# Performance work log

Measured on AMD Instinct MI355X. Metric: run time of the kernel, lower is better.

Reference implementation:

```python
import jax, jax.numpy as jnp
import numpy as np

EMB_DIM = 1024
NUM_HEADS = 16
HEAD_DIM = EMB_DIM // NUM_HEADS
B, S_Q, S_KV = 4, 2048, 2048


def setup_inputs() -> dict:
    key = jax.random.key(0)
    ks = jax.random.split(key, 12)
    s = EMB_DIM ** -0.5  # torch Linear default init scale (approx, uniform-like)
    inp = {
        "q": jax.random.normal(ks[0], (B, S_Q, EMB_DIM), jnp.float32),
        "k": jax.random.normal(ks[1], (B, S_KV, EMB_DIM), jnp.float32),
        "v": jax.random.normal(ks[2], (B, S_KV, EMB_DIM), jnp.float32),
        "mask": jax.random.randint(ks[3], (B, S_KV), 0, 2, jnp.int32),
        "Wq": jax.random.normal(ks[4], (EMB_DIM, EMB_DIM), jnp.float32) * s,
        "bq": jnp.zeros((EMB_DIM,), jnp.float32),
        "Wk": jax.random.normal(ks[5], (EMB_DIM, EMB_DIM), jnp.float32) * s,
        "bk": jnp.zeros((EMB_DIM,), jnp.float32),
        "Wv": jax.random.normal(ks[6], (EMB_DIM, EMB_DIM), jnp.float32) * s,
        "bv": jnp.zeros((EMB_DIM,), jnp.float32),
        "Wo": jax.random.normal(ks[7], (EMB_DIM, EMB_DIM), jnp.float32) * s,
        "bo": jnp.zeros((EMB_DIM,), jnp.float32),
    }
    return inp


def reference(q, k, v, mask, Wq, bq, Wk, bk, Wv, bv, Wo, bo):
    Bsz, Sq, E = q.shape
    Skv = k.shape[1]
    H, D = NUM_HEADS, HEAD_DIM
    scale = D ** -0.5

    # projections (torch Linear: x @ W.T + b)
    qh = (q @ Wq.T + bq).reshape(Bsz, Sq, H, D).transpose(0, 2, 1, 3)   # [B,H,Sq,D]
    kh = (k @ Wk.T + bk).reshape(Bsz, Skv, H, D).transpose(0, 2, 1, 3)  # [B,H,Skv,D]
    vh = (v @ Wv.T + bv).reshape(Bsz, Skv, H, D).transpose(0, 2, 1, 3)  # [B,H,Skv,D]

    attn = jnp.einsum("bhqd,bhkd->bhqk", qh, kh) * scale  # [B,H,Sq,Skv]

    valid = mask != 0                                      # [B,Skv]
    all_invalid = ~jnp.any(valid, axis=-1, keepdims=True)  # [B,1]
    safe = valid | all_invalid                             # reopened rows
    attn = jnp.where(safe[:, None, None, :], attn, -jnp.inf)

    attn = jax.nn.softmax(attn, axis=-1)
    attn = jnp.where(all_invalid.reshape(Bsz, 1, 1, 1), 0.0, attn)

    out = jnp.einsum("bhqk,bhkd->bhqd", attn, vh)          # [B,H,Sq,D]
    out = out.transpose(0, 2, 1, 3).reshape(Bsz, Sq, E)
    return out @ Wo.T + bo
```

## Files before the change

kernel.cpp:

```cpp
#include <hip/hip_runtime.h>
#include <hip/hip_bf16.h>

typedef short bh8 __attribute__((ext_vector_type(8)));
typedef float f32x4 __attribute__((ext_vector_type(4)));
typedef float f32x16 __attribute__((ext_vector_type(16)));
typedef float f2 __attribute__((ext_vector_type(2)));
typedef unsigned int uint4v __attribute__((ext_vector_type(4)));

#define GLOBAL_P(p) ((const __attribute__((address_space(1))) void*)(p))
#define LDS_P(p)    ((__attribute__((address_space(3))) void*)(p))

__device__ inline bh8 pack8(const float4& a, const float4& b) {
    union { bh8 v; __hip_bfloat16 h[8]; } u;
    u.h[0] = __float2bfloat16(a.x); u.h[1] = __float2bfloat16(a.y);
    u.h[2] = __float2bfloat16(a.z); u.h[3] = __float2bfloat16(a.w);
    u.h[4] = __float2bfloat16(b.x); u.h[5] = __float2bfloat16(b.y);
    u.h[6] = __float2bfloat16(b.z); u.h[7] = __float2bfloat16(b.w);
    return u.v;
}

__global__ __launch_bounds__(256) void prep(
    const float* __restrict__ q, const float* __restrict__ Wq,
    const float* __restrict__ Wk, const float* __restrict__ Wv,
    const float* __restrict__ Wo, const int* __restrict__ mask,
    __hip_bfloat16* __restrict__ qbf, __hip_bfloat16* __restrict__ Wb,
    int* __restrict__ idx, int* __restrict__ nv)
{
    __shared__ int ts[256];
    const int bid = blockIdx.x, tid = threadIdx.x;
    if (bid < 4096) {
        size_t i = ((size_t)bid * 256 + tid) * 8;
        float4 x0 = *(const float4*)(q + i), x1 = *(const float4*)(q + i + 4);
        *(bh8*)(qbf + i) = pack8(x0, x1);
    } else if (bid < 6144) {
        const int sb = bid - 4096;
        const int seg = sb >> 9;
        const float* src = (seg == 0) ? Wq : (seg == 1) ? Wk : (seg == 2) ? Wv : Wo;
        size_t i = ((size_t)(sb & 511) * 256 + tid) * 8;
        float4 x0 = *(const float4*)(src + i), x1 = *(const float4*)(src + i + 4);
        *(bh8*)(Wb + (size_t)seg * 1048576 + i) = pack8(x0, x1);
    } else {
        const int b = bid - 6144;
        int f[8], cnt = 0;
#pragma unroll
        for (int j = 0; j < 8; ++j) {
            f[j] = (mask[b * 2048 + tid * 8 + j] != 0) ? 1 : 0;
            cnt += f[j];
        }
        ts[tid] = cnt;
        __syncthreads();
        for (int off = 1; off < 256; off <<= 1) {
            int v = (tid >= off) ? ts[tid - off] : 0;
            __syncthreads();
            ts[tid] += v;
            __syncthreads();
        }
        int base = ts[tid] - cnt;
#pragma unroll
        for (int j = 0; j < 8; ++j)
            if (f[j]) idx[b * 2048 + base++] = tid * 8 + j;
        if (tid == 255) nv[b] = ts[255];
    }
}

__global__ __launch_bounds__(256) void gatherTok(
    const float* __restrict__ kf, const float* __restrict__ vf,
    const int* __restrict__ idx, const int* __restrict__ nv,
    __hip_bfloat16* __restrict__ kc, __hip_bfloat16* __restrict__ vc)
{
    const int b = blockIdx.x >> 7, rb = blockIdx.x & 127;
    const int n = nv[b], np = (n + 127) & ~127;
    const int r = rb * 16 + (threadIdx.x >> 4);
    if (r >= np) return;
    const int c0 = (threadIdx.x & 15) * 64;
    bh8* dk = (bh8*)(kc + ((size_t)b * 2048 + r) * 1024 + c0);
    bh8* dv = (bh8*)(vc + ((size_t)b * 2048 + r) * 1024 + c0);
    if (r < n) {
        const int s = idx[b * 2048 + r];
        const float4* sk = (const float4*)(kf + ((size_t)b * 2048 + s) * 1024 + c0);
        const float4* sv = (const float4*)(vf + ((size_t)b * 2048 + s) * 1024 + c0);
#pragma unroll
        for (int i = 0; i < 8; ++i) {
            dk[i] = pack8(sk[2 * i], sk[2 * i + 1]);
            dv[i] = pack8(sv[2 * i], sv[2 * i + 1]);
        }
    } else {
        bh8 z = {};
#pragma unroll
        for (int i = 0; i < 8; ++i) { dk[i] = z; dv[i] = z; }
    }
}

template <typename TC, bool COMPACT>
__device__ __forceinline__ void gemm_core(
    const __hip_bfloat16* __restrict__ A, const __hip_bfloat16* __restrict__ W,
    const float* __restrict__ bias, TC* __restrict__ C,
    int N, int Ksz, float oscale, const int* __restrict__ nvp,
    int bm, int bn, __hip_bfloat16* As, __hip_bfloat16* Bs)
{
    if constexpr (COMPACT) {
        const int np = (nvp[bm >> 4] + 127) & ~127;
        if ((bm & 15) * 128 >= np) return;
    }
    const int tid = threadIdx.x;
    const int l = tid & 63, w = tid >> 6;
    const int g4 = l >> 4, rl = l & 15;
    const long m0 = (long)bm * 128, n0 = (long)bn * 128;

    const __hip_bfloat16* ag[4];
    const __hip_bfloat16* wg[4];
    int ldsbase[4];
#pragma unroll
    for (int i = 0; i < 4; ++i) {
        int c = i * 256 + tid;
        int row = c >> 3, c8 = c & 7;
        ag[i] = A + (m0 + row) * Ksz + c8 * 8;
        wg[i] = W + (n0 + row) * Ksz + c8 * 8;
        ldsbase[i] = (i * 256 + w * 64) * 8;
    }

    const int wr = w >> 1, wc = w & 1;
    f32x4 acc[4][4];
#pragma unroll
    for (int i = 0; i < 4; ++i)
#pragma unroll
        for (int j = 0; j < 4; ++j) acc[i][j] = f32x4{0.f, 0.f, 0.f, 0.f};

    const int nk = Ksz >> 6;
    for (int t = 0; t < nk; ++t) {
        __syncthreads();
#pragma unroll
        for (int i = 0; i < 4; ++i) {
            __builtin_amdgcn_global_load_lds(GLOBAL_P(ag[i]), LDS_P(As + ldsbase[i]), 16, 0, 0);
            __builtin_amdgcn_global_load_lds(GLOBAL_P(wg[i]), LDS_P(Bs + ldsbase[i]), 16, 0, 0);
            ag[i] += 64; wg[i] += 64;
        }
        __syncthreads();
#pragma unroll
        for (int kc = 0; kc < 2; ++kc) {
            bh8 af[4], bf[4];
#pragma unroll
            for (int mt = 0; mt < 4; ++mt) {
                int row = wr * 64 + mt * 16 + rl;
                af[mt] = *(const bh8*)(As + row * 64 + 8 * g4 + 32 * kc);
            }
#pragma unroll
            for (int nt = 0; nt < 4; ++nt) {
                int row = wc * 64 + nt * 16 + rl;
                bf[nt] = *(const bh8*)(Bs + row * 64 + 8 * g4 + 32 * kc);
            }
#pragma unroll
            for (int mt = 0; mt < 4; ++mt)
#pragma unroll
                for (int nt = 0; nt < 4; ++nt)
                    acc[mt][nt] = __builtin_amdgcn_mfma_f32_16x16x32_bf16(af[mt], bf[nt], acc[mt][nt], 0, 0, 0);
        }
    }

    float bv[4];
#pragma unroll
    for (int nt = 0; nt < 4; ++nt)
        bv[nt] = bias[n0 + wc * 64 + nt * 16 + rl];
#pragma unroll
    for (int mt = 0; mt < 4; ++mt) {
#pragma unroll
        for (int r = 0; r < 4; ++r) {
            long row = m0 + wr * 64 + mt * 16 + g4 * 4 + r;
            TC* cp = C + row * N + n0 + wc * 64 + rl;
#pragma unroll
            for (int nt = 0; nt < 4; ++nt) {
                float x = (acc[mt][nt][r] + bv[nt]) * oscale;
                if constexpr (__is_same(TC, float)) cp[nt * 16] = x;
                else cp[nt * 16] = __float2bfloat16(x);
            }
        }
    }
}

template <typename TC, bool COMPACT>
__global__ __launch_bounds__(256) void gemm_bt(
    const __hip_bfloat16* __restrict__ A, const __hip_bfloat16* __restrict__ W,
    const float* __restrict__ bias, TC* __restrict__ C,
    int N, int Ksz, float oscale, const int* __restrict__ nvp)
{
    __shared__ __hip_bfloat16 As[128 * 64];
    __shared__ __hip_bfloat16 Bs[128 * 64];
    const int nb = N >> 7;
    gemm_core<TC, COMPACT>(A, W, bias, C, N, Ksz, oscale, nvp,
                           blockIdx.x / nb, blockIdx.x % nb, As, Bs);
}

__global__ __launch_bounds__(256) void gemm_projqk(
    const __hip_bfloat16* __restrict__ Aq, const __hip_bfloat16* __restrict__ Ak,
    const __hip_bfloat16* __restrict__ Wb, const float* __restrict__ bq,
    const float* __restrict__ bk, __hip_bfloat16* __restrict__ Cq,
    __hip_bfloat16* __restrict__ Ck, const int* __restrict__ nvp, float csc)
{
    __shared__ __hip_bfloat16 As[128 * 64];
    __shared__ __hip_bfloat16 Bs[128 * 64];
    const int bid = blockIdx.x;
    if (bid < 512)
        gemm_core<__hip_bfloat16, false>(Aq, Wb, bq, Cq, 1024, 1024, csc, nullptr,
                                         bid >> 3, bid & 7, As, Bs);
    else
        gemm_core<__hip_bfloat16, true>(Ak, Wb + 1048576, bk, Ck, 1024, 1024, 1.0f, nvp,
                                        (bid - 512) >> 3, bid & 7, As, Bs);
}

#define THRL 11.0f

__global__ __launch_bounds__(256, 2) void attn_kernel(
    const __hip_bfloat16* __restrict__ Qm, const __hip_bfloat16* __restrict__ Km,
    const __hip_bfloat16* __restrict__ Vm, const int* __restrict__ nvp,
    __hip_bfloat16* __restrict__ Om)
{
    __shared__ __hip_bfloat16 Kt[2][64 * 64];
    __shared__ __hip_bfloat16 Vt[2][64 * 64];
    __shared__ float biasS[2048];
    const int tid = threadIdx.x;
    const int w = tid >> 6, l = tid & 63;
    const int G = l >> 5, c = l & 31;
    const int id = blockIdx.x;
    const int xcd = id & 7, slot = id >> 3;
    const int bh = xcd * 8 + (slot >> 4);
    const int qb = slot & 15;
    const int b = bh >> 4, h = bh & 15;
    const int q0 = qb * 128 + w * 32;

    const int n = nvp[b];
    const int nt = (n + 63) >> 6;

#pragma unroll
    for (int i = 0; i < 8; ++i) {
        int idx = i * 256 + tid;
        biasS[idx] = (idx < n) ? 0.f : -1e30f;
    }

    const __hip_bfloat16* qp = Qm + (size_t)(b * 2048 + q0 + c) * 1024 + h * 64 + 8 * G;
    bh8 qf[4];
#pragma unroll
    for (int kc = 0; kc < 4; ++kc) qf[kc] = *(const bh8*)(qp + 16 * kc);

    const int l38 = l >> 3, lc8 = l & 7;
    const __hip_bfloat16* kg0 = Km + (size_t)(b * 2048 + 16 * w + l38) * 1024 + h * 64 + 8 * ((lc8 ^ l38 ^ (2 * w)) & 7);
    const __hip_bfloat16* kg1 = Km + (size_t)(b * 2048 + 16 * w + 8 + l38) * 1024 + h * 64 + 8 * ((lc8 ^ l38 ^ (2 * w + 1)) & 7);
    const int kbase_e = w * 1024;

    const int vpi = tid >> 3, vd0 = (tid & 7) * 8;
    const __hip_bfloat16* vbase = Vm + (size_t)(b * 2048 + 2 * vpi) * 1024 + h * 64 + vd0;

    bh8 va0, va1;
    auto loadV = [&](int tt) {
        const __hip_bfloat16* vp = vbase + (size_t)tt * 64 * 1024;
        va0 = *(const bh8*)vp;
        va1 = *(const bh8*)(vp + 1024);
    };
    auto stageV = [&](int buf) {
        __hip_bfloat16* dst = &Vt[buf][0];
#pragma unroll
        for (int j = 0; j < 8; ++j) {
            int d = vd0 + j;
            int swz = ((d & 7) ^ (d >> 3)) << 3;
            unsigned lo = (unsigned short)((const short*)&va0)[j];
            unsigned hi = (unsigned short)((const short*)&va1)[j];
            *(unsigned*)&dst[(d * 64 + 2 * vpi) ^ swz] = lo | (hi << 16);
        }
    };
    auto stageK = [&](int buf, int tt) {
        const size_t off = (size_t)tt * 64 * 1024;
        __builtin_amdgcn_global_load_lds(GLOBAL_P(kg0 + off), LDS_P(&Kt[buf][0] + kbase_e), 16, 0, 0);
        __builtin_amdgcn_global_load_lds(GLOBAL_P(kg1 + off), LDS_P(&Kt[buf][0] + kbase_e + 512), 16, 0, 0);
    };

    stageK(0, 0);
    loadV(0);
    stageV(0);
    loadV(nt > 1 ? 1 : 0);
    __syncthreads();

    f32x16 o0 = {0.f}, o1 = {0.f};
    float m_run = -1e29f, l_run = 0.f;

    for (int t = 0; t < nt; ++t) {
        const int buf = t & 1;
        if (t < nt - 1) {
            stageK(buf ^ 1, t + 1);
            stageV(buf ^ 1);
            loadV(t + 2 < nt ? t + 2 : nt - 1);
        }
        __builtin_amdgcn_sched_barrier(0);

        const __hip_bfloat16* kbuf = &Kt[buf][0];
        const int kx0 = ((c & 7) ^ (c >> 3)) << 3;
        const int kx1 = kx0 ^ 32;
        f32x16 s0 = {0.f}, s1 = {0.f};
        __builtin_amdgcn_s_setprio(1);
#pragma unroll
        for (int kc = 0; kc < 4; ++kc) {
            bh8 kf = *(const bh8*)(kbuf + c * 64 + ((16 * kc + 8 * G) ^ kx0));
            s0 = __builtin_amdgcn_mfma_f32_32x32x16_bf16(kf, qf[kc], s0, 0, 0, 0);
        }
#pragma unroll
        for (int kc = 0; kc < 4; ++kc) {
            bh8 kf = *(const bh8*)(kbuf + (c + 32) * 64 + ((16 * kc + 8 * G) ^ kx1));
            s1 = __builtin_amdgcn_mfma_f32_32x32x16_bf16(kf, qf[kc], s1, 0, 0, 0);
        }
        __builtin_amdgcn_s_setprio(0);

        f2 mx2 = {-1e30f, -1e30f};
#pragma unroll
        for (int ct = 0; ct < 2; ++ct) {
            f2* sp = (f2*)(ct ? &s1 : &s0);
#pragma unroll
            for (int i2 = 0; i2 < 8; ++i2) {
                const int i = i2 * 2;
                f2 bb = *(const f2*)&biasS[t * 64 + ct * 32 + (i >> 2) * 8 + 4 * G + (i & 3)];
                f2 sv = sp[i2] + bb;
                sp[i2] = sv;
                mx2 = __builtin_elementwise_max(mx2, sv);
            }
        }
        float mxl = fmaxf(mx2[0], mx2[1]);

        if (__all(mxl - m_run <= THRL)) {
            f2 ls2 = {0.f, 0.f};
            f2 m2 = {m_run, m_run};
#pragma unroll
            for (int ct = 0; ct < 2; ++ct) {
                f2* sp = (f2*)(ct ? &s1 : &s0);
#pragma unroll
                for (int i2 = 0; i2 < 8; ++i2) {
                    f2 e = sp[i2] - m2;
                    f2 p;
                    p[0] = __builtin_amdgcn_exp2f(e[0]);
                    p[1] = __builtin_amdgcn_exp2f(e[1]);
                    sp[i2] = p; ls2 += p;
                }
            }
            l_run += ls2[0] + ls2[1];
        } else {
            float mxf = fmaxf(mxl, __shfl_xor(mxl, 32));
            const float m_new = fmaxf(m_run, mxf);
            const float fac = __builtin_amdgcn_exp2f(m_run - m_new);
            f2 ls2 = {0.f, 0.f};
            f2 m2 = {m_new, m_new};
#pragma unroll
            for (int ct = 0; ct < 2; ++ct) {
                f2* sp = (f2*)(ct ? &s1 : &s0);
#pragma unroll
                for (int i2 = 0; i2 < 8; ++i2) {
                    f2 e = sp[i2] - m2;
                    f2 p;
                    p[0] = __builtin_amdgcn_exp2f(e[0]);
                    p[1] = __builtin_amdgcn_exp2f(e[1]);
                    sp[i2] = p; ls2 += p;
                }
            }
            l_run = l_run * fac + (ls2[0] + ls2[1]);
            m_run = m_new;
            f2 fc = {fac, fac};
            f2* o0p = (f2*)&o0; f2* o1p = (f2*)&o1;
#pragma unroll
            for (int i2 = 0; i2 < 8; ++i2) { o0p[i2] *= fc; o1p[i2] *= fc; }
        }

        const __hip_bfloat16* vbuf = &Vt[buf][0];
        const int swz0 = ((c & 7) ^ (c >> 3)) << 3;
        const int swz1 = ((c & 7) ^ ((c + 32) >> 3)) << 3;
#pragma unroll
        for (int sl = 0; sl < 4; ++sl) {
            const f32x16& ps = (sl < 2) ? s0 : s1;
            const int R0 = 8 * (sl & 1);
            unsigned a0, a1, b0, b1;
            asm("v_cvt_pk_bf16_f32 %0, %1, %2" : "=v"(a0) : "v"(ps[R0 + 0]), "v"(ps[R0 + 1]));
            asm("v_cvt_pk_bf16_f32 %0, %1, %2" : "=v"(a1) : "v"(ps[R0 + 2]), "v"(ps[R0 + 3]));
            asm("v_cvt_pk_bf16_f32 %0, %1, %2" : "=v"(b0) : "v"(ps[R0 + 4]), "v"(ps[R0 + 5]));
            asm("v_cvt_pk_bf16_f32 %0, %1, %2" : "=v"(b1) : "v"(ps[R0 + 6]), "v"(ps[R0 + 7]));
            asm("v_permlane32_swap_b32 %0, %1" : "+v"(a0), "+v"(b0));
            asm("v_permlane32_swap_b32 %0, %1" : "+v"(a1), "+v"(b1));
            uint4v pu = {a0, a1, b0, b1};
            bh8 pf = __builtin_bit_cast(bh8, pu);
            const int kvb = 16 * sl + 8 * G;
            bh8 vf0 = *(const bh8*)(vbuf + c * 64 + (kvb ^ swz0));
            bh8 vf1 = *(const bh8*)(vbuf + (c + 32) * 64 + (kvb ^ swz1));
            __builtin_amdgcn_s_setprio(1);
            o0 = __builtin_amdgcn_mfma_f32_32x32x16_bf16(vf0, pf, o0, 0, 0, 0);
            o1 = __builtin_amdgcn_mfma_f32_32x32x16_bf16(vf1, pf, o1, 0, 0, 0);
            __builtin_amdgcn_s_setprio(0);
        }

        __syncthreads();
    }

    float l_tot = l_run + __shfl_xor(l_run, 32);
    float inv = (l_tot > 0.f) ? 1.f / l_tot : 0.f;
    __hip_bfloat16* op = Om + (size_t)(b * 2048 + q0 + c) * 1024 + h * 64 + 4 * G;
#pragma unroll
    for (int dt = 0; dt < 2; ++dt) {
#pragma unroll
        for (int rb = 0; rb < 4; ++rb) {
            union { ushort4 u; __hip_bfloat16 hv[4]; } cv;
#pragma unroll
            for (int j = 0; j < 4; ++j) {
                float x = (dt ? o1[rb * 4 + j] : o0[rb * 4 + j]) * inv;
                cv.hv[j] = __float2bfloat16(x);
            }
            *(ushort4*)(op + dt * 32 + rb * 8) = cv.u;
        }
    }
}

extern "C" void kernel_launch(void* const* d_in, const int* in_sizes, int n_in,
                              void* d_out, int out_size, void* d_ws, size_t ws_size,
                              hipStream_t stream) {
    const float* q  = (const float*)d_in[0];
    const float* k  = (const float*)d_in[1];
    const float* v  = (const float*)d_in[2];
    const int*   mk = (const int*)d_in[3];
    const float* Wq = (const float*)d_in[4];
    const float* bq = (const float*)d_in[5];
    const float* Wk = (const float*)d_in[6];
    const float* bk = (const float*)d_in[7];
    const float* Wv = (const float*)d_in[8];
    const float* bv = (const float*)d_in[9];
    const float* Wo = (const float*)d_in[10];
    const float* bo = (const float*)d_in[11];
    float* out = (float*)d_out;

    const float CSC = 0.18033688011112042f;
    const size_t MN = (size_t)8192 * 1024;
    const size_t WN = (size_t)1024 * 1024;
    __hip_bfloat16* R0 = (__hip_bfloat16*)d_ws;
    __hip_bfloat16* R1 = R0 + MN;
    __hip_bfloat16* R2 = R1 + MN;
    __hip_bfloat16* R3 = R2 + MN;
    __hip_bfloat16* Wb = R3 + MN;
    int* idxp = (int*)(Wb + 4 * WN);
    int* nvp  = idxp + 4 * 2048;
    __hip_bfloat16* R4 = (__hip_bfloat16*)((char*)idxp + 33024);

    prep<<<6148, 256, 0, stream>>>(q, Wq, Wk, Wv, Wo, mk, R0, Wb, idxp, nvp);
    gatherTok<<<512, 256, 0, stream>>>(k, v, idxp, nvp, R1, R2);
    gemm_projqk<<<1024, 256, 0, stream>>>(R0, R1, Wb, bq, bk, R3, R4, nvp, CSC);
    gemm_bt<__hip_bfloat16, true><<<512, 256, 0, stream>>>(R2, Wb + 2 * WN, bv, R1, 1024, 1024, 1.0f, nvp);
    attn_kernel<<<1024, 256, 0, stream>>>(R3, R4, R1, nvp, R0);
    gemm_bt<float, false><<<512, 256, 0, stream>>>(R0, Wb + 3 * WN, bo, out, 1024, 1024, 1.0f, nullptr);
}
```

Baseline: 203.6 us.

## Fuse mask compaction with K/V gather and merge QKV projection launches

```diff
diff --git a/kernel.cpp b/kernel.cpp
--- a/kernel.cpp
+++ b/kernel.cpp
@@ -23,10 +23,13 @@
     const float* __restrict__ q, const float* __restrict__ Wq,
     const float* __restrict__ Wk, const float* __restrict__ Wv,
     const float* __restrict__ Wo, const int* __restrict__ mask,
+    const float* __restrict__ kf, const float* __restrict__ vf,
     __hip_bfloat16* __restrict__ qbf, __hip_bfloat16* __restrict__ Wb,
-    int* __restrict__ idx, int* __restrict__ nv)
+    __hip_bfloat16* __restrict__ kc, __hip_bfloat16* __restrict__ vc,
+    int* __restrict__ nv)
 {
     __shared__ int ts[256];
+    __shared__ int idxL[2048];
     const int bid = blockIdx.x, tid = threadIdx.x;
     if (bid < 4096) {
         size_t i = ((size_t)bid * 256 + tid) * 8;
@@ -40,7 +43,8 @@
         float4 x0 = *(const float4*)(src + i), x1 = *(const float4*)(src + i + 4);
         *(bh8*)(Wb + (size_t)seg * 1048576 + i) = pack8(x0, x1);
     } else {
-        const int b = bid - 6144;
+        const int gb = bid - 6144;
+        const int b = gb >> 7, rb = gb & 127;
         int f[8], cnt = 0;
 #pragma unroll
         for (int j = 0; j < 8; ++j) {
@@ -58,36 +62,31 @@
         int base = ts[tid] - cnt;
 #pragma unroll
         for (int j = 0; j < 8; ++j)
-            if (f[j]) idx[b * 2048 + base++] = tid * 8 + j;
-        if (tid == 255) nv[b] = ts[255];
-    }
-}
-
-__global__ __launch_bounds__(256) void gatherTok(
-    const float* __restrict__ kf, const float* __restrict__ vf,
-    const int* __restrict__ idx, const int* __restrict__ nv,
-    __hip_bfloat16* __restrict__ kc, __hip_bfloat16* __restrict__ vc)
-{
-    const int b = blockIdx.x >> 7, rb = blockIdx.x & 127;
-    const int n = nv[b], np = (n + 127) & ~127;
-    const int r = rb * 16 + (threadIdx.x >> 4);
-    if (r >= np) return;
-    const int c0 = (threadIdx.x & 15) * 64;
-    bh8* dk = (bh8*)(kc + ((size_t)b * 2048 + r) * 1024 + c0);
-    bh8* dv = (bh8*)(vc + ((size_t)b * 2048 + r) * 1024 + c0);
-    if (r < n) {
-        const int s = idx[b * 2048 + r];
-        const float4* sk = (const float4*)(kf + ((size_t)b * 2048 + s) * 1024 + c0);
-        const float4* sv = (const float4*)(vf + ((size_t)b * 2048 + s) * 1024 + c0);
-#pragma unroll
-        for (int i = 0; i < 8; ++i) {
-            dk[i] = pack8(sk[2 * i], sk[2 * i + 1]);
-            dv[i] = pack8(sv[2 * i], sv[2 * i + 1]);
-        }
-    } else {
-        bh8 z = {};
-#pragma unroll
-        for (int i = 0; i < 8; ++i) { dk[i] = z; dv[i] = z; }
+            if (f[j]) idxL[base++] = tid * 8 + j;
+        const int n = ts[255];
+        if (rb == 0 && tid == 255) nv[b] = n;
+        __syncthreads();
+
+        const int np = (n + 127) & ~127;
+        const int r = rb * 16 + (tid >> 4);
+        if (r >= np) return;
+        const int c0 = (tid & 15) * 64;
+        bh8* dk = (bh8*)(kc + ((size_t)b * 2048 + r) * 1024 + c0);
+        bh8* dv = (bh8*)(vc + ((size_t)b * 2048 + r) * 1024 + c0);
+        if (r < n) {
+            const int s = idxL[r];
+            const float4* sk = (const float4*)(kf + ((size_t)b * 2048 + s) * 1024 + c0);
+            const float4* sv = (const float4*)(vf + ((size_t)b * 2048 + s) * 1024 + c0);
+#pragma unroll
+            for (int i = 0; i < 8; ++i) {
+                dk[i] = pack8(sk[2 * i], sk[2 * i + 1]);
+                dv[i] = pack8(sv[2 * i], sv[2 * i + 1]);
+            }
+        } else {
+            bh8 z = {};
+#pragma unroll
+            for (int i = 0; i < 8; ++i) { dk[i] = z; dv[i] = z; }
+        }
     }
 }
 
@@ -205,6 +204,28 @@
     else
         gemm_core<__hip_bfloat16, true>(Ak, Wb + 1048576, bk, Ck, 1024, 1024, 1.0f, nvp,
                                         (bid - 512) >> 3, bid & 7, As, Bs);
+}
+
+__global__ __launch_bounds__(256) void gemm_projqkv(
+    const __hip_bfloat16* __restrict__ Aq, const __hip_bfloat16* __restrict__ Ak,
+    const __hip_bfloat16* __restrict__ Av, const __hip_bfloat16* __restrict__ Wb,
+    const float* __restrict__ bq, const float* __restrict__ bk,
+    const float* __restrict__ bv, __hip_bfloat16* __restrict__ Cq,
+    __hip_bfloat16* __restrict__ Ck, __hip_bfloat16* __restrict__ Cv,
+    const int* __restrict__ nvp, float csc)
+{
+    __shared__ __hip_bfloat16 As[128 * 64];
+    __shared__ __hip_bfloat16 Bs[128 * 64];
+    const int bid = blockIdx.x;
+    if (bid < 512)
+        gemm_core<__hip_bfloat16, false>(Aq, Wb, bq, Cq, 1024, 1024, csc, nullptr,
+                                         bid >> 3, bid & 7, As, Bs);
+    else if (bid < 1024)
+        gemm_core<__hip_bfloat16, true>(Ak, Wb + 1048576, bk, Ck, 1024, 1024, 1.0f, nvp,
+                                        (bid - 512) >> 3, bid & 7, As, Bs);
+    else
+        gemm_core<__hip_bfloat16, true>(Av, Wb + 2097152, bv, Cv, 1024, 1024, 1.0f, nvp,
+                                        (bid - 1024) >> 3, bid & 7, As, Bs);
 }
 
 #define THRL 11.0f
@@ -435,14 +456,19 @@
     __hip_bfloat16* R2 = R1 + MN;
     __hip_bfloat16* R3 = R2 + MN;
     __hip_bfloat16* Wb = R3 + MN;
-    int* idxp = (int*)(Wb + 4 * WN);
-    int* nvp  = idxp + 4 * 2048;
-    __hip_bfloat16* R4 = (__hip_bfloat16*)((char*)idxp + 33024);
-
-    prep<<<6148, 256, 0, stream>>>(q, Wq, Wk, Wv, Wo, mk, R0, Wb, idxp, nvp);
-    gatherTok<<<512, 256, 0, stream>>>(k, v, idxp, nvp, R1, R2);
-    gemm_projqk<<<1024, 256, 0, stream>>>(R0, R1, Wb, bq, bk, R3, R4, nvp, CSC);
-    gemm_bt<__hip_bfloat16, true><<<512, 256, 0, stream>>>(R2, Wb + 2 * WN, bv, R1, 1024, 1024, 1.0f, nvp);
-    attn_kernel<<<1024, 256, 0, stream>>>(R3, R4, R1, nvp, R0);
+    int* nvp = (int*)(Wb + 4 * WN);
+    __hip_bfloat16* R4 = (__hip_bfloat16*)((char*)nvp + 256);
+    __hip_bfloat16* R5 = R4 + MN;
+    const size_t need = (size_t)((char*)(R5 + MN) - (char*)d_ws);
+
+    prep<<<6656, 256, 0, stream>>>(q, Wq, Wk, Wv, Wo, mk, k, v, R0, Wb, R1, R2, nvp);
+    if (ws_size >= need) {
+        gemm_projqkv<<<1536, 256, 0, stream>>>(R0, R1, R2, Wb, bq, bk, bv, R3, R4, R5, nvp, CSC);
+        attn_kernel<<<1024, 256, 0, stream>>>(R3, R4, R5, nvp, R0);
+    } else {
+        gemm_projqk<<<1024, 256, 0, stream>>>(R0, R1, Wb, bq, bk, R3, R4, nvp, CSC);
+        gemm_bt<__hip_bfloat16, true><<<512, 256, 0, stream>>>(R2, Wb + 2 * WN, bv, R1, 1024, 1024, 1.0f, nvp);
+        attn_kernel<<<1024, 256, 0, stream>>>(R3, R4, R1, nvp, R0);
+    }
     gemm_bt<float, false><<<512, 256, 0, stream>>>(R0, Wb + 3 * WN, bo, out, 1024, 1024, 1.0f, nullptr);
 }
```

Measured after the change: 205.6 us. No clear change (+1.0%).
